# Kernel optimization log

Hardware: AMD Instinct MI355X
Metric: run time of the kernel (lower is better)

## Reference

```python
import jax, jax.numpy as jnp
import numpy as np

S, N, C, E, L = 4, 50000, 256, 800000, 3
EPS = 1e-5  # nn.LayerNorm default eps


def setup_inputs() -> dict:
    key = jax.random.key(0)
    ks = jax.random.split(key, 10)
    sc = 1.0 / np.sqrt(C)
    x = jax.random.normal(ks[0], (S, N, C), jnp.float32)
    edge_index = jax.random.randint(ks[1], (S, 2, E), 0, N, dtype=jnp.int32)
    edge_weight = jax.random.uniform(ks[2], (S, E), jnp.float32)
    W_gcn = jax.random.uniform(ks[3], (L, C, C), jnp.float32, -sc, sc)
    b_gcn = jnp.zeros((L, C), jnp.float32)
    ln_scale = jnp.ones((L, C), jnp.float32)
    ln_bias = jnp.zeros((L, C), jnp.float32)
    w_ih = jax.random.uniform(ks[4], (3 * C, C), jnp.float32, -sc, sc)
    w_hh = jax.random.uniform(ks[5], (3 * C, C), jnp.float32, -sc, sc)
    b_ih = jax.random.uniform(ks[6], (3 * C,), jnp.float32, -sc, sc)
    b_hh = jax.random.uniform(ks[7], (3 * C,), jnp.float32, -sc, sc)
    return dict(x=x, edge_index=edge_index, edge_weight=edge_weight,
                W_gcn=W_gcn, b_gcn=b_gcn, ln_scale=ln_scale, ln_bias=ln_bias,
                w_ih=w_ih, w_hh=w_hh, b_ih=b_ih, b_hh=b_hh)


def _gcn_conv(h, row, col, ew, W, b):
    """PyG GCNConv: out = D^{-1/2} (A + I) D^{-1/2} (h W) + b, edge weights ew."""
    h = h @ W  # [N, C]
    loop = jnp.arange(N, dtype=row.dtype)
    row = jnp.concatenate([row, loop])
    col = jnp.concatenate([col, loop])
    ew = jnp.concatenate([ew, jnp.ones((N,), ew.dtype)])
    deg = jax.ops.segment_sum(ew, col, num_segments=N)  # in-degree at targets
    dinv = jnp.where(deg > 0, jax.lax.rsqrt(jnp.maximum(deg, EPS * 0 + 1e-12)), 0.0)
    norm = dinv[row] * ew * dinv[col]  # [E+N]
    msg = h[row] * norm[:, None]       # gather from sources
    return jax.ops.segment_sum(msg, col, num_segments=N) + b


def _layernorm(h, scale, bias):
    mu = jnp.mean(h, axis=-1, keepdims=True)
    var = jnp.mean(jnp.square(h - mu), axis=-1, keepdims=True)
    return (h - mu) * jax.lax.rsqrt(var + EPS) * scale + bias


def _snapshot(x, ei, ew, W_gcn, b_gcn, ln_scale, ln_bias):
    h = x
    row, col = ei[0], ei[1]
    for l in range(L):
        h = _gcn_conv(h, row, col, ew, W_gcn[l], b_gcn[l])
        h = _layernorm(h, ln_scale[l], ln_bias[l])
        h = jax.nn.relu(h)  # dropout is identity in eval mode
    return h


def _gru_last(seq, w_ih, w_hh, b_ih, b_hh):
    """seq: [S, N, C] -> final hidden [N, C] (torch single-layer GRU)."""
    def step(h, x_t):
        gi = x_t @ w_ih.T + b_ih
        gh = h @ w_hh.T + b_hh
        i_r, i_z, i_n = jnp.split(gi, 3, axis=-1)
        h_r, h_z, h_n = jnp.split(gh, 3, axis=-1)
        r = jax.nn.sigmoid(i_r + h_r)
        z = jax.nn.sigmoid(i_z + h_z)
        n = jnp.tanh(i_n + r * h_n)
        return (1.0 - z) * n + z * h, None
    h0 = jnp.zeros(seq.shape[1:], seq.dtype)
    h_last, _ = jax.lax.scan(step, h0, seq)
    return h_last


def reference(x, edge_index, edge_weight, W_gcn, b_gcn, ln_scale, ln_bias,
              w_ih, w_hh, b_ih, b_hh):
    feats = jax.vmap(lambda xs, eis, ews: _snapshot(xs, eis, ews, W_gcn, b_gcn, ln_scale, ln_bias))(
        x, edge_index, edge_weight)  # [S, N, C]
    return _gru_last(feats, w_ih, w_hh, b_ih, b_hh)  # [N, C]
```

## Files before the change

kernel.cpp:

```cpp
#include <hip/hip_runtime.h>
#include <cmath>

#define S_ 4
#define N_ 50000
#define C_ 256
#define E_ 800000
#define L_ 3
#define EPS_ 1e-5f
#define CAP_ 64
#define NSHARD_ 8
#define SHARD_N_ (N_ / NSHARD_)

typedef __attribute__((ext_vector_type(8))) short bf16x8;
typedef __attribute__((ext_vector_type(4))) float f32x4;

__device__ __forceinline__ float bf2f(unsigned short s) {
  return __uint_as_float(((unsigned)s) << 16);
}
__device__ __forceinline__ unsigned short f2bf(float f) {
  unsigned u = __float_as_uint(f);
  return (unsigned short)((u + 0x7fffu + ((u >> 16) & 1u)) >> 16);
}

__device__ __forceinline__ void gload_lds16(const void* g, void* l) {
  __builtin_amdgcn_global_load_lds(
      (const __attribute__((address_space(1))) unsigned int*)g,
      (__attribute__((address_space(3))) unsigned int*)l, 16, 0, 0);
}

__device__ __forceinline__ void swz_block(int id, int nbx, int nby, int& bmi, int& bni) {
  const int NB8 = nby * 8;
  int fullb = (nbx >> 3) * NB8;
  if (id < fullb) {
    int g = id / NB8, pp = id - g * NB8;
    bmi = g * 8 + (pp & 7);
    bni = pp >> 3;
  } else {
    int rem = nbx & 7;
    int idp = id - fullb;
    bmi = (nbx & ~7) + idp % rem;
    bni = idp / rem;
  }
}

template<bool AF32>
__global__ __launch_bounds__(256) void gemm_bf16_kernel(
    const unsigned short* __restrict__ A, const float* __restrict__ Af,
    const unsigned short* __restrict__ Bt,
    unsigned short* __restrict__ Cout, int M, int Nn, int K, int nby)
{
  __shared__ alignas(16) unsigned short As[2][128 * 32];
  __shared__ alignas(16) unsigned short Bs[2][128 * 32];
  const int tid = threadIdx.x;
  const int lane = tid & 63;
  const int wid = tid >> 6;
  const int wr = wid >> 1, wc = wid & 1;
  int bmi, bni;
  swz_block(blockIdx.x, gridDim.x / nby, nby, bmi, bni);
  const int bm = bmi * 128, bn = bni * 128;
  const int l15 = lane & 15, l4 = lane >> 4;

  f32x4 acc[4][4] = {};

  int offA[4], offB[4];
  #pragma unroll
  for (int mi = 0; mi < 4; ++mi) {
    int ra = wr * 64 + mi * 16 + l15;
    offA[mi] = ra * 32 + ((l4 ^ ((ra >> 1) & 3)) << 3);
    int rb = wc * 64 + mi * 16 + l15;
    offB[mi] = rb * 32 + ((l4 ^ ((rb >> 1) & 3)) << 3);
  }
  const int rs = tid >> 2;
  const int gs = tid & 3;

  float4 fa[2][2];

  auto loadA_f32 = [&](int k0) {
    #pragma unroll
    for (int t2 = 0; t2 < 2; ++t2) {
      int r = rs + t2 * 64;
      int q = gs ^ ((r >> 1) & 3);
      int arow = bm + r; if (arow >= M) arow = M - 1;
      const float* srcp = &Af[(size_t)arow * K + k0 + q * 8];
      fa[t2][0] = *(const float4*)srcp;
      fa[t2][1] = *(const float4*)(srcp + 4);
    }
  };
  auto writeA_f32 = [&](int buf) {
    #pragma unroll
    for (int t2 = 0; t2 < 2; ++t2) {
      int slot = t2 * 256 + tid;
      union { unsigned short us[8]; bf16x8 v; } u;
      const float* f = (const float*)&fa[t2][0];
      #pragma unroll
      for (int j = 0; j < 8; ++j) u.us[j] = f2bf(f[j]);
      *(bf16x8*)&As[buf][slot * 8] = u.v;
    }
  };
  auto stageA_bf = [&](int buf, int k0) {
    #pragma unroll
    for (int t2 = 0; t2 < 2; ++t2) {
      int r = rs + t2 * 64;
      int q = gs ^ ((r >> 1) & 3);
      int arow = bm + r; if (arow >= M) arow = M - 1;
      gload_lds16(&A[(size_t)arow * K + k0 + q * 8], &As[buf][(t2 * 256 + tid) * 8]);
    }
  };
  auto stageB = [&](int buf, int k0) {
    #pragma unroll
    for (int t2 = 0; t2 < 2; ++t2) {
      int r = rs + t2 * 64;
      int q = gs ^ ((r >> 1) & 3);
      gload_lds16(&Bt[(size_t)(bn + r) * K + k0 + q * 8], &Bs[buf][(t2 * 256 + tid) * 8]);
    }
  };

  const int nt = K >> 5;
  if constexpr (AF32) {
    loadA_f32(0);
    stageB(0, 0);
    writeA_f32(0);
  } else {
    stageA_bf(0, 0);
    stageB(0, 0);
  }
  asm volatile("s_waitcnt vmcnt(0)" ::: "memory");
  __syncthreads();

  int cur = 0;
  for (int t = 0; t < nt; ++t) {
    if (t + 1 < nt) {
      if constexpr (AF32) {
        loadA_f32((t + 1) * 32);
        stageB(cur ^ 1, (t + 1) * 32);
      } else {
        stageA_bf(cur ^ 1, (t + 1) * 32);
        stageB(cur ^ 1, (t + 1) * 32);
      }
    }

    bf16x8 af[4], bfr[4];
    #pragma unroll
    for (int mi = 0; mi < 4; ++mi) af[mi] = *(const bf16x8*)&As[cur][offA[mi]];
    #pragma unroll
    for (int ni = 0; ni < 4; ++ni) bfr[ni] = *(const bf16x8*)&Bs[cur][offB[ni]];
    #pragma unroll
    for (int mi = 0; mi < 4; ++mi)
      #pragma unroll
      for (int ni = 0; ni < 4; ++ni)
        acc[mi][ni] = __builtin_amdgcn_mfma_f32_16x16x32_bf16(
            bfr[ni], af[mi], acc[mi][ni], 0, 0, 0);

    if constexpr (AF32) {
      if (t + 1 < nt) writeA_f32(cur ^ 1);
    }
    asm volatile("s_waitcnt vmcnt(0)" ::: "memory");
    __syncthreads();
    cur ^= 1;
  }

  #pragma unroll
  for (int mi = 0; mi < 4; ++mi) {
    int row = bm + wr * 64 + mi * 16 + l15;
    if (row < M) {
      #pragma unroll
      for (int ni = 0; ni < 4; ++ni) {
        int colb = bn + wc * 64 + ni * 16 + l4 * 4;
        ushort4 o;
        o.x = f2bf(acc[mi][ni][0]);
        o.y = f2bf(acc[mi][ni][1]);
        o.z = f2bf(acc[mi][ni][2]);
        o.w = f2bf(acc[mi][ni][3]);
        *(ushort4*)&Cout[(size_t)row * Nn + colb] = o;
      }
    }
  }
}

__global__ __launch_bounds__(256) void gru_fused_kernel(
    const unsigned short* __restrict__ feat,
    const unsigned short* __restrict__ hq_in,
    const unsigned short* __restrict__ Wp_ih,
    const unsigned short* __restrict__ Wp_hh,
    const float* __restrict__ b_ih, const float* __restrict__ b_hh,
    unsigned short* __restrict__ hq_out, float* __restrict__ hout,
    int first, int M)
{
  __shared__ alignas(16) unsigned short As[2][128 * 32];
  __shared__ alignas(16) unsigned short Bs[2][96 * 32];
  const int tid = threadIdx.x;
  const int lane = tid & 63;
  const int wv = tid >> 6;
  const int l15 = lane & 15, l4 = lane >> 4;

  int bmi, bni;
  swz_block(blockIdx.x, gridDim.x / 8, 8, bmi, bni);
  const int bm = bmi * 128;
  const int c0 = bni * 32;
  const int brow0 = bni * 96;

  f32x4 acc_i[2][6] = {};
  f32x4 acc_h[2][6] = {};

  int offA[2], offB[6];
  #pragma unroll
  for (int mi = 0; mi < 2; ++mi) {
    int ra = wv * 32 + mi * 16 + l15;
    offA[mi] = ra * 32 + ((l4 ^ ((ra >> 1) & 3)) << 3);
  }
  #pragma unroll
  for (int ni = 0; ni < 6; ++ni) {
    int rb = ni * 16 + l15;
    offB[ni] = rb * 32 + ((l4 ^ ((rb >> 1) & 3)) << 3);
  }

  const int nt = first ? 8 : 16;

  auto stage = [&](int buf, int t) {
    int k0 = (t & 7) * 32;
    const unsigned short* Ap = (t < 8) ? feat : hq_in;
    const unsigned short* Bp = (t < 8) ? Wp_ih : Wp_hh;
    #pragma unroll
    for (int t2 = 0; t2 < 2; ++t2) {
      int slot = t2 * 256 + tid;
      int r = slot >> 2;
      int q = (slot & 3) ^ ((r >> 1) & 3);
      int arow = bm + r; if (arow >= M) arow = M - 1;
      gload_lds16(&Ap[(size_t)arow * 256 + k0 + q * 8], &As[buf][slot * 8]);
    }
    {
      int slot = tid;
      int r = slot >> 2;
      int q = (slot & 3) ^ ((r >> 1) & 3);
      gload_lds16(&Bp[(size_t)(brow0 + r) * 256 + k0 + q * 8], &Bs[buf][slot * 8]);
    }
    if (tid < 128) {
      int slot = 256 + tid;
      int r = slot >> 2;
      int q = (slot & 3) ^ ((r >> 1) & 3);
      gload_lds16(&Bp[(size_t)(brow0 + r) * 256 + k0 + q * 8], &Bs[buf][slot * 8]);
    }
  };

  stage(0, 0);
  asm volatile("s_waitcnt vmcnt(0)" ::: "memory");
  __syncthreads();

  int cur = 0;
  for (int t = 0; t < nt; ++t) {
    if (t + 1 < nt) stage(cur ^ 1, t + 1);

    bf16x8 af[2], bfr[6];
    #pragma unroll
    for (int mi = 0; mi < 2; ++mi) af[mi] = *(const bf16x8*)&As[cur][offA[mi]];
    #pragma unroll
    for (int ni = 0; ni < 6; ++ni) bfr[ni] = *(const bf16x8*)&Bs[cur][offB[ni]];
    if (t < 8) {
      #pragma unroll
      for (int mi = 0; mi < 2; ++mi)
        #pragma unroll
        for (int ni = 0; ni < 6; ++ni)
          acc_i[mi][ni] = __builtin_amdgcn_mfma_f32_16x16x32_bf16(
              bfr[ni], af[mi], acc_i[mi][ni], 0, 0, 0);
    } else {
      #pragma unroll
      for (int mi = 0; mi < 2; ++mi)
        #pragma unroll
        for (int ni = 0; ni < 6; ++ni)
          acc_h[mi][ni] = __builtin_amdgcn_mfma_f32_16x16x32_bf16(
              bfr[ni], af[mi], acc_h[mi][ni], 0, 0, 0);
    }

    asm volatile("s_waitcnt vmcnt(0)" ::: "memory");
    __syncthreads();
    cur ^= 1;
  }

  #pragma unroll
  for (int mi = 0; mi < 2; ++mi) {
    int row = bm + wv * 32 + mi * 16 + l15;
    if (row < M) {
      #pragma unroll
      for (int cni = 0; cni < 2; ++cni) {
        int c = c0 + cni * 16 + l4 * 4;
        float4 bir = *(const float4*)&b_ih[c];
        float4 biz = *(const float4*)&b_ih[256 + c];
        float4 bin = *(const float4*)&b_ih[512 + c];
        float4 bhr = *(const float4*)&b_hh[c];
        float4 bhz = *(const float4*)&b_hh[256 + c];
        float4 bhn = *(const float4*)&b_hh[512 + c];
        float hpv[4] = {0.f, 0.f, 0.f, 0.f};
        if (!first) {
          ushort4 hp = *(const ushort4*)&hq_in[(size_t)row * 256 + c];
          hpv[0] = bf2f(hp.x); hpv[1] = bf2f(hp.y);
          hpv[2] = bf2f(hp.z); hpv[3] = bf2f(hp.w);
        }
        const float* pbir = (const float*)&bir; const float* pbiz = (const float*)&biz;
        const float* pbin = (const float*)&bin; const float* pbhr = (const float*)&bhr;
        const float* pbhz = (const float*)&bhz; const float* pbhn = (const float*)&bhn;
        float hv[4];
        #pragma unroll
        for (int rr = 0; rr < 4; ++rr) {
          float gir = acc_i[mi][0 + cni][rr] + pbir[rr];
          float giz = acc_i[mi][2 + cni][rr] + pbiz[rr];
          float gin = acc_i[mi][4 + cni][rr] + pbin[rr];
          float ghr = (first ? 0.f : acc_h[mi][0 + cni][rr]) + pbhr[rr];
          float ghz = (first ? 0.f : acc_h[mi][2 + cni][rr]) + pbhz[rr];
          float ghn = (first ? 0.f : acc_h[mi][4 + cni][rr]) + pbhn[rr];
          float rg = 1.f / (1.f + expf(-(gir + ghr)));
          float zg = 1.f / (1.f + expf(-(giz + ghz)));
          float ng = tanhf(gin + rg * ghn);
          hv[rr] = (1.f - zg) * ng + zg * hpv[rr];
        }
        if (hq_out) {
          ushort4 o;
          o.x = f2bf(hv[0]); o.y = f2bf(hv[1]); o.z = f2bf(hv[2]); o.w = f2bf(hv[3]);
          *(ushort4*)&hq_out[(size_t)row * 256 + c] = o;
        }
        if (hout) {
          float4 o = make_float4(hv[0], hv[1], hv[2], hv[3]);
          *(float4*)&hout[(size_t)row * 256 + c] = o;
        }
      }
    }
  }
}

__global__ void prep_weights_kernel(const float* __restrict__ W_gcn,
                                    const float* __restrict__ w_ih,
                                    const float* __restrict__ w_hh,
                                    unsigned short* __restrict__ wt_gcn,
                                    unsigned short* __restrict__ wp_ih,
                                    unsigned short* __restrict__ wp_hh) {
  int i = blockIdx.x * blockDim.x + threadIdx.x;
  const int LCC = L_ * C_ * C_, WSZ = 768 * C_;
  if (i < LCC) {
    int l = i / (C_ * C_);
    int rem = i - l * C_ * C_;
    int nn = rem >> 8, k = rem & 255;
    wt_gcn[i] = f2bf(W_gcn[l * C_ * C_ + k * C_ + nn]);
  } else if (i < LCC + 2 * WSZ) {
    int j = i - LCC;
    int which = j / WSZ;
    int d = j - which * WSZ;
    int jrow = d >> 8, k = d & 255;
    int chunk = jrow / 96, jj = jrow - chunk * 96;
    int g = jj >> 5, dc = jj & 31;
    int srow = g * 256 + chunk * 32 + dc;
    float v = which ? w_hh[srow * 256 + k] : w_ih[srow * 256 + k];
    (which ? wp_hh : wp_ih)[d] = f2bf(v);
  }
}

__global__ __launch_bounds__(256) void scatter_fill_kernel(
    const int* __restrict__ edge_idx, const float* __restrict__ edge_w,
    unsigned int* __restrict__ recs, int* __restrict__ cnt_g) {
  const int tid = threadIdx.x;
  const int shard = blockIdx.x & (NSHARD_ - 1);
  const int bidx = blockIdx.x >> 3;
  const int nblk = gridDim.x >> 3;
  const int lo = shard * SHARD_N_, hi = lo + SHARD_N_;
  for (int s = 0; s < S_; ++s) {
    const int* row = edge_idx + (size_t)s * 2 * E_;
    const int* col = row + E_;
    const float* ew = edge_w + (size_t)s * E_;
    for (int e = bidx * 256 + tid; e < E_; e += nblk * 256) {
      int c = col[e];
      if (c >= lo && c < hi) {
        int ng = s * N_ + c;
        int pos = atomicAdd(&cnt_g[ng], 1);
        if (pos < CAP_) {
          recs[((size_t)ng << 6) + pos] =
              (unsigned int)row[e] | ((unsigned int)f2bf(ew[e]) << 16);
        }
      }
    }
  }
}

__global__ __launch_bounds__(256) void deg_dinv_kernel(
    const unsigned int* __restrict__ recs, const int* __restrict__ cnt_g,
    float* __restrict__ dinv_g) {
  const int lane = threadIdx.x & 63, wv = threadIdx.x >> 6;
  const int ng = blockIdx.x * 4 + wv;
  int cnt = min(cnt_g[ng], CAP_);
  float w = 0.f;
  if (lane < cnt)
    w = bf2f((unsigned short)(recs[((size_t)ng << 6) + lane] >> 16));
  #pragma unroll
  for (int off = 32; off > 0; off >>= 1) w += __shfl_xor(w, off);
  if (lane == 0) dinv_g[ng] = rsqrtf(w + 1.0f);
}

__global__ void normify_kernel(unsigned int* __restrict__ recs,
                               const int* __restrict__ cnt_g,
                               const float* __restrict__ dinv_g) {
  int idx = blockIdx.x * blockDim.x + threadIdx.x;
  if (idx < S_ * N_ * CAP_) {
    int ng = idx >> 6, slot = idx & 63;
    int cnt = min(cnt_g[ng], CAP_);
    if (slot < cnt) {
      unsigned int rec = recs[idx];
      int src = (int)(rec & 0xFFFFu);
      float w = bf2f((unsigned short)(rec >> 16));
      int s = ng / N_;
      float nrm = dinv_g[s * N_ + src] * w * dinv_g[ng];
      recs[idx] = (rec & 0xFFFFu) | ((unsigned int)f2bf(nrm) << 16);
    }
  }
}

__global__ __launch_bounds__(256) void spmm_ln_relu_kernel(
    const unsigned short* __restrict__ hW_all, const int* __restrict__ cnt_g,
    const unsigned int* __restrict__ src_norm, const float* __restrict__ dinv_g,
    const float* __restrict__ bgcn, const float* __restrict__ lnsc,
    const float* __restrict__ lnbi, unsigned short* __restrict__ out)
{
  const int tid = threadIdx.x;
  const int lane = tid & 63, wv = tid >> 6;
  const int n_g = blockIdx.x * 4 + wv;
  const int s = n_g / N_;
  const int n = n_g - s * N_;
  const int c4 = lane << 2;
  const unsigned short* hW = hW_all + ((size_t)s * N_ << 8);

  const int cnt = min(cnt_g[n_g], CAP_);
  unsigned int rec = (lane < cnt) ? src_norm[((size_t)n_g << 6) + lane] : 0u;

  float a0, a1, a2, a3;
  {
    float dv = dinv_g[n_g];
    float w = dv * dv;
    ushort4 u = *(const ushort4*)&hW[((size_t)n << 8) + c4];
    a0 = w * bf2f(u.x); a1 = w * bf2f(u.y); a2 = w * bf2f(u.z); a3 = w * bf2f(u.w);
  }
  int j = 0;
  for (; j + 3 < cnt; j += 4) {
    unsigned int r0 = __shfl((int)rec, j + 0);
    unsigned int r1 = __shfl((int)rec, j + 1);
    unsigned int r2 = __shfl((int)rec, j + 2);
    unsigned int r3 = __shfl((int)rec, j + 3);
    ushort4 u0 = *(const ushort4*)&hW[((size_t)(r0 & 0xFFFFu) << 8) + c4];
    ushort4 u1 = *(const ushort4*)&hW[((size_t)(r1 & 0xFFFFu) << 8) + c4];
    ushort4 u2 = *(const ushort4*)&hW[((size_t)(r2 & 0xFFFFu) << 8) + c4];
    ushort4 u3 = *(const ushort4*)&hW[((size_t)(r3 & 0xFFFFu) << 8) + c4];
    float n0 = bf2f((unsigned short)(r0 >> 16));
    float n1 = bf2f((unsigned short)(r1 >> 16));
    float n2 = bf2f((unsigned short)(r2 >> 16));
    float n3 = bf2f((unsigned short)(r3 >> 16));
    a0 = fmaf(n0, bf2f(u0.x), a0); a1 = fmaf(n0, bf2f(u0.y), a1);
    a2 = fmaf(n0, bf2f(u0.z), a2); a3 = fmaf(n0, bf2f(u0.w), a3);
    a0 = fmaf(n1, bf2f(u1.x), a0); a1 = fmaf(n1, bf2f(u1.y), a1);
    a2 = fmaf(n1, bf2f(u1.z), a2); a3 = fmaf(n1, bf2f(u1.w), a3);
    a0 = fmaf(n2, bf2f(u2.x), a0); a1 = fmaf(n2, bf2f(u2.y), a1);
    a2 = fmaf(n2, bf2f(u2.z), a2); a3 = fmaf(n2, bf2f(u2.w), a3);
    a0 = fmaf(n3, bf2f(u3.x), a0); a1 = fmaf(n3, bf2f(u3.y), a1);
    a2 = fmaf(n3, bf2f(u3.z), a2); a3 = fmaf(n3, bf2f(u3.w), a3);
  }
  for (; j < cnt; ++j) {
    unsigned int r0 = __shfl((int)rec, j);
    ushort4 u0 = *(const ushort4*)&hW[((size_t)(r0 & 0xFFFFu) << 8) + c4];
    float n0 = bf2f((unsigned short)(r0 >> 16));
    a0 = fmaf(n0, bf2f(u0.x), a0); a1 = fmaf(n0, bf2f(u0.y), a1);
    a2 = fmaf(n0, bf2f(u0.z), a2); a3 = fmaf(n0, bf2f(u0.w), a3);
  }

  float4 bg = *(const float4*)&bgcn[c4];
  float v0 = a0 + bg.x, v1 = a1 + bg.y, v2 = a2 + bg.z, v3 = a3 + bg.w;
  float s1 = (v0 + v1) + (v2 + v3);
  float s2 = (v0 * v0 + v1 * v1) + (v2 * v2 + v3 * v3);
  #pragma unroll
  for (int off = 32; off > 0; off >>= 1) {
    s1 += __shfl_xor(s1, off);
    s2 += __shfl_xor(s2, off);
  }
  float mu = s1 * (1.0f / C_);
  float var = s2 * (1.0f / C_) - mu * mu;
  float inv = rsqrtf(var + EPS_);
  float4 sc = *(const float4*)&lnsc[c4];
  float4 bi = *(const float4*)&lnbi[c4];
  ushort4 o;
  o.x = f2bf(fmaxf((v0 - mu) * inv * sc.x + bi.x, 0.f));
  o.y = f2bf(fmaxf((v1 - mu) * inv * sc.y + bi.y, 0.f));
  o.z = f2bf(fmaxf((v2 - mu) * inv * sc.z + bi.z, 0.f));
  o.w = f2bf(fmaxf((v3 - mu) * inv * sc.w + bi.w, 0.f));
  *(ushort4*)&out[((size_t)n_g << 8) + c4] = o;
}

extern "C" void kernel_launch(void* const* d_in, const int* in_sizes, int n_in,
                              void* d_out, int out_size, void* d_ws, size_t ws_size,
                              hipStream_t stream) {
  const float* x        = (const float*)d_in[0];
  const int*   edge_idx = (const int*)d_in[1];
  const float* edge_w   = (const float*)d_in[2];
  const float* W_gcn    = (const float*)d_in[3];
  const float* b_gcn    = (const float*)d_in[4];
  const float* ln_scale = (const float*)d_in[5];
  const float* ln_bias  = (const float*)d_in[6];
  const float* w_ih     = (const float*)d_in[7];
  const float* w_hh     = (const float*)d_in[8];
  const float* b_ih     = (const float*)d_in[9];
  const float* b_hh     = (const float*)d_in[10];
  float* h_out = (float*)d_out;

  char* p = (char*)d_ws;
  auto carve = [&](size_t bytes) -> void* {
    void* r = (void*)p;
    p += (bytes + 255) & ~(size_t)255;
    return r;
  };
  unsigned int* recs = (unsigned int*)carve((size_t)S_ * N_ * CAP_ * 4);
  int*   cnt_g       = (int*)carve((size_t)S_ * N_ * 4);
  float* dinv_g      = (float*)carve((size_t)S_ * N_ * 4);
  unsigned short* wt_gcn = (unsigned short*)carve((size_t)L_ * C_ * C_ * 2);
  unsigned short* wp_ih  = (unsigned short*)carve((size_t)768 * C_ * 2);
  unsigned short* wp_hh  = (unsigned short*)carve((size_t)768 * C_ * 2);
  unsigned short* hW_all = (unsigned short*)carve((size_t)S_ * N_ * C_ * 2);
  unsigned short* fA_all = (unsigned short*)carve((size_t)S_ * N_ * C_ * 2);
  unsigned short* fB_all = (unsigned short*)carve((size_t)S_ * N_ * C_ * 2);
  unsigned short* hq0    = (unsigned short*)carve((size_t)N_ * C_ * 2);
  unsigned short* hq1    = (unsigned short*)carve((size_t)N_ * C_ * 2);

  const int TB = 256;

  hipMemsetAsync(cnt_g, 0, (size_t)S_ * N_ * 4, stream);

  const int PREP_N = L_ * C_ * C_ + 2 * 768 * C_;
  prep_weights_kernel<<<(PREP_N + TB - 1) / TB, TB, 0, stream>>>(
      W_gcn, w_ih, w_hh, wt_gcn, wp_ih, wp_hh);

  scatter_fill_kernel<<<2048, TB, 0, stream>>>(edge_idx, edge_w, recs, cnt_g);
  deg_dinv_kernel<<<S_ * N_ / 4, TB, 0, stream>>>(recs, cnt_g, dinv_g);
  normify_kernel<<<(S_ * N_ * CAP_ + TB - 1) / TB, TB, 0, stream>>>(
      recs, cnt_g, dinv_g);

  const int M_all = S_ * N_;
  const int nbx = (M_all + 127) / 128;
  {
    unsigned short* louts[3] = {fA_all, fB_all, fA_all};
    const unsigned short* hin = nullptr;
    for (int l = 0; l < L_; ++l) {
      if (l == 0) {
        gemm_bf16_kernel<true><<<nbx * (C_ / 128), 256, 0, stream>>>(
            nullptr, x, wt_gcn, hW_all, M_all, C_, C_, C_ / 128);
      } else {
        gemm_bf16_kernel<false><<<nbx * (C_ / 128), 256, 0, stream>>>(
            hin, nullptr, wt_gcn + (size_t)l * C_ * C_, hW_all, M_all, C_, C_, C_ / 128);
      }
      spmm_ln_relu_kernel<<<M_all / 4, 256, 0, stream>>>(
          hW_all, cnt_g, recs, dinv_g, b_gcn + l * C_,
          ln_scale + l * C_, ln_bias + l * C_, louts[l]);
      hin = louts[l];
    }
  }
  const unsigned short* feat_all = fA_all;

  const int gnb = ((N_ + 127) / 128) * 8;
  unsigned short* hq_cur = hq0;
  unsigned short* hq_nxt = hq1;
  for (int s = 0; s < S_; ++s) {
    bool last = (s == S_ - 1);
    gru_fused_kernel<<<gnb, 256, 0, stream>>>(
        feat_all + (size_t)s * N_ * C_,
        hq_cur,
        wp_ih, wp_hh, b_ih, b_hh,
        last ? nullptr : hq_nxt,
        last ? h_out : nullptr,
        (s == 0) ? 1 : 0, N_);
    unsigned short* t = hq_cur; hq_cur = hq_nxt; hq_nxt = t;
  }
}
```

Before: 1.482 ms.

## Chunk hW into column slabs and split SpMM from LayerNorm

The GEMM now writes hW in a chunked column-major layout: 8 slabs of 32 channels, each holding all rows. The SpMM kernel is restructured so each block works on one slab, which keeps the per-slab gather working set (about 3.2MB per snapshot) cache-resident. The kernel writes fp32 partial sums to a new pacc buffer, and a separate kernel applies bias, LayerNorm and ReLU. The trade-off is an extra fp32 round trip through a 200MB buffer per layer and narrower 4-byte gathers per lane.

```diff
diff --git a/kernel.cpp b/kernel.cpp
--- a/kernel.cpp
+++ b/kernel.cpp
@@ -10,6 +10,7 @@
 #define CAP_ 64
 #define NSHARD_ 8
 #define SHARD_N_ (N_ / NSHARD_)
+#define CHC_ 32
 
 typedef __attribute__((ext_vector_type(8))) short bf16x8;
 typedef __attribute__((ext_vector_type(4))) float f32x4;
@@ -165,13 +166,14 @@
     if (row < M) {
       #pragma unroll
       for (int ni = 0; ni < 4; ++ni) {
-        int colb = bn + wc * 64 + ni * 16 + l4 * 4;
+        int col = bn + wc * 64 + ni * 16 + l4 * 4;
+        int chunk = col >> 5, coff = col & 31;
         ushort4 o;
         o.x = f2bf(acc[mi][ni][0]);
         o.y = f2bf(acc[mi][ni][1]);
         o.z = f2bf(acc[mi][ni][2]);
         o.w = f2bf(acc[mi][ni][3]);
-        *(ushort4*)&Cout[(size_t)row * Nn + colb] = o;
+        *(ushort4*)&Cout[((size_t)chunk * M + row) * CHC_ + coff] = o;
       }
     }
   }
@@ -410,63 +412,58 @@
   }
 }
 
-__global__ __launch_bounds__(256) void spmm_ln_relu_kernel(
-    const unsigned short* __restrict__ hW_all, const int* __restrict__ cnt_g,
-    const unsigned int* __restrict__ src_norm, const float* __restrict__ dinv_g,
-    const float* __restrict__ bgcn, const float* __restrict__ lnsc,
-    const float* __restrict__ lnbi, unsigned short* __restrict__ out)
+__global__ __launch_bounds__(256) void spmm_partial_kernel(
+    const unsigned short* __restrict__ hW_cm, const int* __restrict__ cnt_g,
+    const unsigned int* __restrict__ recs, const float* __restrict__ dinv_g,
+    float* __restrict__ pacc, int M)
 {
-  const int tid = threadIdx.x;
-  const int lane = tid & 63, wv = tid >> 6;
-  const int n_g = blockIdx.x * 4 + wv;
-  const int s = n_g / N_;
-  const int n = n_g - s * N_;
+  const int ch = blockIdx.x & 7;
+  const int bid = blockIdx.x >> 3;
+  const int nblk = gridDim.x >> 3;
+  const int lane = threadIdx.x & 63, wv = threadIdx.x >> 6;
+  const int g16 = lane >> 4, l16 = lane & 15;
+
+  for (int s = 0; s < S_; ++s) {
+    const unsigned short* slab = hW_cm + ((size_t)ch * M + (size_t)s * N_) * CHC_;
+    for (int n0 = bid * 16; n0 < N_; n0 += nblk * 16) {
+      int n = n0 + wv * 4 + g16;
+      int ng = s * N_ + n;
+      int cnt = min(cnt_g[ng], CAP_);
+      float a0 = 0.f, a1 = 0.f;
+      unsigned int rec = 0;
+      for (int j = 0; j < cnt; ++j) {
+        if ((j & 15) == 0) rec = recs[((size_t)ng << 6) + (j & 48) + l16];
+        unsigned int r = (unsigned int)__shfl((int)rec, (g16 << 4) | (j & 15));
+        unsigned int src = r & 0xFFFFu;
+        float nrm = bf2f((unsigned short)(r >> 16));
+        unsigned int pair = *(const unsigned int*)&slab[(size_t)src * CHC_ + l16 * 2];
+        a0 = fmaf(nrm, bf2f((unsigned short)(pair & 0xFFFFu)), a0);
+        a1 = fmaf(nrm, bf2f((unsigned short)(pair >> 16)), a1);
+      }
+      {
+        float dv = dinv_g[ng];
+        float w = dv * dv;
+        unsigned int pair = *(const unsigned int*)&slab[(size_t)n * CHC_ + l16 * 2];
+        a0 = fmaf(w, bf2f((unsigned short)(pair & 0xFFFFu)), a0);
+        a1 = fmaf(w, bf2f((unsigned short)(pair >> 16)), a1);
+      }
+      float2 o = make_float2(a0, a1);
+      *(float2*)&pacc[((size_t)ng << 8) + ch * CHC_ + l16 * 2] = o;
+    }
+  }
+}
+
+__global__ __launch_bounds__(256) void ln_relu_kernel(
+    const float* __restrict__ pacc, const float* __restrict__ bgcn,
+    const float* __restrict__ lnsc, const float* __restrict__ lnbi,
+    unsigned short* __restrict__ out)
+{
+  const int lane = threadIdx.x & 63, wv = threadIdx.x >> 6;
+  const int ng = blockIdx.x * 4 + wv;
   const int c4 = lane << 2;
-  const unsigned short* hW = hW_all + ((size_t)s * N_ << 8);
-
-  const int cnt = min(cnt_g[n_g], CAP_);
-  unsigned int rec = (lane < cnt) ? src_norm[((size_t)n_g << 6) + lane] : 0u;
-
-  float a0, a1, a2, a3;
-  {
-    float dv = dinv_g[n_g];
-    float w = dv * dv;
-    ushort4 u = *(const ushort4*)&hW[((size_t)n << 8) + c4];
-    a0 = w * bf2f(u.x); a1 = w * bf2f(u.y); a2 = w * bf2f(u.z); a3 = w * bf2f(u.w);
-  }
-  int j = 0;
-  for (; j + 3 < cnt; j += 4) {
-    unsigned int r0 = __shfl((int)rec, j + 0);
-    unsigned int r1 = __shfl((int)rec, j + 1);
-    unsigned int r2 = __shfl((int)rec, j + 2);
-    unsigned int r3 = __shfl((int)rec, j + 3);
-    ushort4 u0 = *(const ushort4*)&hW[((size_t)(r0 & 0xFFFFu) << 8) + c4];
-    ushort4 u1 = *(const ushort4*)&hW[((size_t)(r1 & 0xFFFFu) << 8) + c4];
-    ushort4 u2 = *(const ushort4*)&hW[((size_t)(r2 & 0xFFFFu) << 8) + c4];
-    ushort4 u3 = *(const ushort4*)&hW[((size_t)(r3 & 0xFFFFu) << 8) + c4];
-    float n0 = bf2f((unsigned short)(r0 >> 16));
-    float n1 = bf2f((unsigned short)(r1 >> 16));
-    float n2 = bf2f((unsigned short)(r2 >> 16));
-    float n3 = bf2f((unsigned short)(r3 >> 16));
-    a0 = fmaf(n0, bf2f(u0.x), a0); a1 = fmaf(n0, bf2f(u0.y), a1);
-    a2 = fmaf(n0, bf2f(u0.z), a2); a3 = fmaf(n0, bf2f(u0.w), a3);
-    a0 = fmaf(n1, bf2f(u1.x), a0); a1 = fmaf(n1, bf2f(u1.y), a1);
-    a2 = fmaf(n1, bf2f(u1.z), a2); a3 = fmaf(n1, bf2f(u1.w), a3);
-    a0 = fmaf(n2, bf2f(u2.x), a0); a1 = fmaf(n2, bf2f(u2.y), a1);
-    a2 = fmaf(n2, bf2f(u2.z), a2); a3 = fmaf(n2, bf2f(u2.w), a3);
-    a0 = fmaf(n3, bf2f(u3.x), a0); a1 = fmaf(n3, bf2f(u3.y), a1);
-    a2 = fmaf(n3, bf2f(u3.z), a2); a3 = fmaf(n3, bf2f(u3.w), a3);
-  }
-  for (; j < cnt; ++j) {
-    unsigned int r0 = __shfl((int)rec, j);
-    ushort4 u0 = *(const ushort4*)&hW[((size_t)(r0 & 0xFFFFu) << 8) + c4];
-    float n0 = bf2f((unsigned short)(r0 >> 16));
-    a0 = fmaf(n0, bf2f(u0.x), a0); a1 = fmaf(n0, bf2f(u0.y), a1);
-    a2 = fmaf(n0, bf2f(u0.z), a2); a3 = fmaf(n0, bf2f(u0.w), a3);
-  }
-
+  float4 a = *(const float4*)&pacc[((size_t)ng << 8) + c4];
   float4 bg = *(const float4*)&bgcn[c4];
-  float v0 = a0 + bg.x, v1 = a1 + bg.y, v2 = a2 + bg.z, v3 = a3 + bg.w;
+  float v0 = a.x + bg.x, v1 = a.y + bg.y, v2 = a.z + bg.z, v3 = a.w + bg.w;
   float s1 = (v0 + v1) + (v2 + v3);
   float s2 = (v0 * v0 + v1 * v1) + (v2 * v2 + v3 * v3);
   #pragma unroll
@@ -484,7 +481,7 @@
   o.y = f2bf(fmaxf((v1 - mu) * inv * sc.y + bi.y, 0.f));
   o.z = f2bf(fmaxf((v2 - mu) * inv * sc.z + bi.z, 0.f));
   o.w = f2bf(fmaxf((v3 - mu) * inv * sc.w + bi.w, 0.f));
-  *(ushort4*)&out[((size_t)n_g << 8) + c4] = o;
+  *(ushort4*)&out[((size_t)ng << 8) + c4] = o;
 }
 
 extern "C" void kernel_launch(void* const* d_in, const int* in_sizes, int n_in,
@@ -512,10 +509,11 @@
   unsigned int* recs = (unsigned int*)carve((size_t)S_ * N_ * CAP_ * 4);
   int*   cnt_g       = (int*)carve((size_t)S_ * N_ * 4);
   float* dinv_g      = (float*)carve((size_t)S_ * N_ * 4);
+  float* pacc        = (float*)carve((size_t)S_ * N_ * C_ * 4);
   unsigned short* wt_gcn = (unsigned short*)carve((size_t)L_ * C_ * C_ * 2);
   unsigned short* wp_ih  = (unsigned short*)carve((size_t)768 * C_ * 2);
   unsigned short* wp_hh  = (unsigned short*)carve((size_t)768 * C_ * 2);
-  unsigned short* hW_all = (unsigned short*)carve((size_t)S_ * N_ * C_ * 2);
+  unsigned short* hW_cm  = (unsigned short*)carve((size_t)S_ * N_ * C_ * 2);
   unsigned short* fA_all = (unsigned short*)carve((size_t)S_ * N_ * C_ * 2);
   unsigned short* fB_all = (unsigned short*)carve((size_t)S_ * N_ * C_ * 2);
   unsigned short* hq0    = (unsigned short*)carve((size_t)N_ * C_ * 2);
@@ -542,14 +540,15 @@
     for (int l = 0; l < L_; ++l) {
       if (l == 0) {
         gemm_bf16_kernel<true><<<nbx * (C_ / 128), 256, 0, stream>>>(
-            nullptr, x, wt_gcn, hW_all, M_all, C_, C_, C_ / 128);
+            nullptr, x, wt_gcn, hW_cm, M_all, C_, C_, C_ / 128);
       } else {
         gemm_bf16_kernel<false><<<nbx * (C_ / 128), 256, 0, stream>>>(
-            hin, nullptr, wt_gcn + (size_t)l * C_ * C_, hW_all, M_all, C_, C_, C_ / 128);
-      }
-      spmm_ln_relu_kernel<<<M_all / 4, 256, 0, stream>>>(
-          hW_all, cnt_g, recs, dinv_g, b_gcn + l * C_,
-          ln_scale + l * C_, ln_bias + l * C_, louts[l]);
+            hin, nullptr, wt_gcn + (size_t)l * C_ * C_, hW_cm, M_all, C_, C_, C_ / 128);
+      }
+      spmm_partial_kernel<<<2048, 256, 0, stream>>>(
+          hW_cm, cnt_g, recs, dinv_g, pacc, M_all);
+      ln_relu_kernel<<<M_all / 4, 256, 0, stream>>>(
+          pacc, b_gcn + l * C_, ln_scale + l * C_, ln_bias + l * C_, louts[l]);
       hin = louts[l];
     }
   }
```

Result: slower. 2.316 ms (+56.3%).
